# Kernel tuning notes

Hardware: AMD Instinct MI355X
Metric: run time of the kernel (lower is better)

## Reference

```python
import jax, jax.numpy as jnp
import numpy as np

N = 50000
E = 600000
F_IN = 128      # float features (in_channels - 1)
CE = 8          # cell embedding dim
D_IN = F_IN + CE  # 136
C = 128         # out_channels
NUM_CELLS = 854
NEG_SLOPE = 0.2
LN_EPS = 1e-5


def _gat_layer(x, src, dst, W, a_src, a_dst, b):
    """PyG GATConv, heads=1, concat=False, add_self_loops already in src/dst.
    x: [N, Din]; src/dst: [Etot]; W: [Din, C]; a_src/a_dst: [C]; b: [C].
    """
    h = x @ W                               # [N, C]
    alpha_src = h @ a_src                   # [N]
    alpha_dst = h @ a_dst                   # [N]
    e = jax.nn.leaky_relu(alpha_src[src] + alpha_dst[dst], NEG_SLOPE)  # [Etot]
    # segment softmax over edges sharing a destination node
    m = jax.ops.segment_max(e, dst, num_segments=N)    # [N] (every node has a self-loop)
    ex = jnp.exp(e - m[dst])                           # [Etot]
    denom = jax.ops.segment_sum(ex, dst, num_segments=N)  # [N]
    alpha = ex / denom[dst]                            # [Etot]
    out = jax.ops.segment_sum(h[src] * alpha[:, None], dst, num_segments=N)  # [N, C]
    return out + b


def _layer_norm(x, g, b):
    mu = jnp.mean(x, axis=-1, keepdims=True)
    var = jnp.var(x, axis=-1, keepdims=True)
    return (x - mu) * jax.lax.rsqrt(var + LN_EPS) * g + b


def setup_inputs() -> dict:
    key = jax.random.key(0)
    ks = jax.random.split(key, 12)
    x_base = jax.random.normal(ks[0], (N, F_IN), dtype=jnp.float32)
    cell_ids = jax.random.randint(ks[1], (N,), 0, NUM_CELLS, dtype=jnp.int64)
    edge_index = jax.random.randint(ks[2], (2, E), 0, N, dtype=jnp.int64)
    s = 0.05
    cell_emb = jax.random.normal(ks[3], (NUM_CELLS, CE), dtype=jnp.float32)
    W1 = jax.random.normal(ks[4], (D_IN, C), dtype=jnp.float32) * s
    a_src1 = jax.random.normal(ks[5], (C,), dtype=jnp.float32) * s
    a_dst1 = jax.random.normal(ks[6], (C,), dtype=jnp.float32) * s
    b1 = jnp.zeros((C,), dtype=jnp.float32)
    ln_g = jnp.ones((C,), dtype=jnp.float32)
    ln_b = jnp.zeros((C,), dtype=jnp.float32)
    W2 = jax.random.normal(ks[7], (C, C), dtype=jnp.float32) * s
    a_src2 = jax.random.normal(ks[8], (C,), dtype=jnp.float32) * s
    a_dst2 = jax.random.normal(ks[9], (C,), dtype=jnp.float32) * s
    b2 = jnp.zeros((C,), dtype=jnp.float32)
    return {
        "x_base": x_base, "cell_ids": cell_ids, "edge_index": edge_index,
        "cell_emb": cell_emb,
        "W1": W1, "a_src1": a_src1, "a_dst1": a_dst1, "b1": b1,
        "ln_g": ln_g, "ln_b": ln_b,
        "W2": W2, "a_src2": a_src2, "a_dst2": a_dst2, "b2": b2,
    }


def reference(x_base, cell_ids, edge_index, cell_emb,
              W1, a_src1, a_dst1, b1, ln_g, ln_b,
              W2, a_src2, a_dst2, b2):
    # embed cell ids and concat (equiv. to x[:, :-1] + Embedding(x[:, -1]))
    x = jnp.concatenate([x_base, cell_emb[cell_ids]], axis=1)   # [N, 136]
    # PyG GATConv adds self-loops internally
    loops = jnp.arange(N, dtype=edge_index.dtype)
    src = jnp.concatenate([edge_index[0], loops])
    dst = jnp.concatenate([edge_index[1], loops])
    # layer 1 + LN + ELU (dropout inactive in eval mode)
    x = _gat_layer(x, src, dst, W1, a_src1, a_dst1, b1)
    x = jax.nn.elu(_layer_norm(x, ln_g, ln_b))
    # layer 2 (no norm/activation on last layer)
    x = _gat_layer(x, src, dst, W2, a_src2, a_dst2, b2)
    return x
```

## Files before the change

### kernel.cpp

```cpp
#include <hip/hip_runtime.h>
#include <hip/hip_fp16.h>
#include <cstdint>
#include <cstddef>

#define NEG_SLOPE 0.2f
#define LN_EPS 1e-5f

constexpr int BS = 256;
constexpr int STRIDE = 96;

typedef _Float16 f16x8 __attribute__((ext_vector_type(8)));
typedef float f32x4 __attribute__((ext_vector_type(4)));

__global__ void k_build(
    const int* __restrict__ esrc, const int* __restrict__ edst,
    int* __restrict__ cnt, unsigned short* __restrict__ sn,
    const float* __restrict__ x, const int* __restrict__ cid,
    const float* __restrict__ emb, _Float16* __restrict__ xb,
    const float* __restrict__ W1, const float* __restrict__ W2,
    _Float16* __restrict__ Wt1, _Float16* __restrict__ Wt2,
    int e, int etot, int n, int npad, int nbE, int xblocks)
{
    int b = blockIdx.x;
    if (b < nbE) {
        int i = b * BS + threadIdx.x;
        if (i >= etot) return;
        int s, d;
        if (i < e) { s = esrc[i]; d = edst[i]; }
        else       { s = d = i - e; }
        int slot = atomicAdd(&cnt[d], 1);
        if (slot < STRIDE)
            sn[d * STRIDE + slot] = (unsigned short)s;
    } else if (b < nbE + xblocks) {
        int r = (b - nbE) * 8 + (threadIdx.x >> 5);
        int c = threadIdx.x & 31;
        if (r >= npad) return;
        _Float16* row = xb + (size_t)r * 160;
        if (r < n) {
            const float* xr = x + (size_t)r * 128;
            #pragma unroll
            for (int k = 0; k < 4; ++k) row[c + 32 * k] = (_Float16)xr[c + 32 * k];
            float v = (c < 8) ? emb[cid[r] * 8 + c] : 0.f;
            row[128 + c] = (_Float16)v;
        } else {
            #pragma unroll
            for (int k = 0; k < 5; ++k) row[c + 32 * k] = (_Float16)0.f;
        }
    } else {
        int idx = (b - nbE - xblocks) * BS + threadIdx.x;
        if (idx < 128 * 160) {
            int nn = idx / 160, k = idx - nn * 160;
            Wt1[idx] = (_Float16)((k < 136) ? W1[(size_t)k * 128 + nn] : 0.f);
        } else if (idx < 128 * 160 + 128 * 128) {
            int j = idx - 128 * 160;
            int nn = j >> 7, k = j & 127;
            Wt2[j] = (_Float16)W2[(size_t)k * 128 + nn];
        }
    }
}

template<int KP>
__global__ __launch_bounds__(256) void k_gemm_mfma(
    const _Float16* __restrict__ A, const _Float16* __restrict__ Bt,
    const float* __restrict__ a_src, const float* __restrict__ a_dst,
    _Float16* __restrict__ hb, float* __restrict__ as_,
    float* __restrict__ ad_, int n)
{
    __shared__ float red[2][16][2][2];
    int tid = threadIdx.x;
    int wave = tid >> 6, lane = tid & 63;
    int rg = wave >> 1, ch = wave & 1;
    int r15 = lane & 15, q = lane >> 4;
    int rowBase = blockIdx.x * 32 + rg * 16;
    int colBase = ch * 64;

    f32x4 acc[4] = {};

    const _Float16* Wp[4];
    #pragma unroll
    for (int s = 0; s < 4; ++s)
        Wp[s] = Bt + (size_t)(colBase + s * 16 + r15) * KP + q * 8;
    const _Float16* Xp = A + (size_t)(rowBase + r15) * KP + q * 8;

    #pragma unroll
    for (int k0 = 0; k0 < KP; k0 += 32) {
        f16x8 wv[4];
        #pragma unroll
        for (int s = 0; s < 4; ++s) wv[s] = *(const f16x8*)(Wp[s] + k0);
        f16x8 xv = *(const f16x8*)(Xp + k0);
        #pragma unroll
        for (int s = 0; s < 4; ++s)
            acc[s] = __builtin_amdgcn_mfma_f32_16x16x32_f16(wv[s], xv, acc[s], 0, 0, 0);
    }

    int row = rowBase + r15;
    bool ok = row < n;
    float vs = 0.f, vd = 0.f;
    #pragma unroll
    for (int s = 0; s < 4; ++s) {
        float4 as4 = *(const float4*)&a_src[colBase + s * 16 + q * 4];
        float4 ad4 = *(const float4*)&a_dst[colBase + s * 16 + q * 4];
        f32x4 d = acc[s];
        vs += d[0]*as4.x + d[1]*as4.y + d[2]*as4.z + d[3]*as4.w;
        vd += d[0]*ad4.x + d[1]*ad4.y + d[2]*ad4.z + d[3]*ad4.w;
        if (ok) {
            ushort4 u;
            u.x = __half_as_ushort(__float2half_rn(d[0]));
            u.y = __half_as_ushort(__float2half_rn(d[1]));
            u.z = __half_as_ushort(__float2half_rn(d[2]));
            u.w = __half_as_ushort(__float2half_rn(d[3]));
            *(ushort4*)&hb[(size_t)row * 128 + colBase + s * 16 + q * 4] = u;
        }
    }
    vs += __shfl_xor(vs, 16); vs += __shfl_xor(vs, 32);
    vd += __shfl_xor(vd, 16); vd += __shfl_xor(vd, 32);
    if (q == 0) { red[rg][r15][ch][0] = vs; red[rg][r15][ch][1] = vd; }
    __syncthreads();
    if (ch == 0 && q == 0 && ok) {
        as_[row] = red[rg][r15][0][0] + red[rg][r15][1][0];
        ad_[row] = red[rg][r15][0][1] + red[rg][r15][1][1];
    }
}

template<bool LN_ELU, bool OUT_HALF>
__global__ __launch_bounds__(256) void k_agg(
    const _Float16* __restrict__ hb, const unsigned short* __restrict__ sn,
    const int* __restrict__ cnt, const float* __restrict__ as_,
    const float* __restrict__ ad_, const float* __restrict__ bias,
    const float* __restrict__ ln_g, const float* __restrict__ ln_b,
    void* __restrict__ outv, int n_nodes)
{
    int wave = threadIdx.x >> 6, lane = threadIdx.x & 63;
    int n = blockIdx.x * 4 + wave;
    if (n >= n_nodes) return;
    int len = cnt[n];
    len = len < STRIDE ? len : STRIDE;
    len = __builtin_amdgcn_readfirstlane(len);
    int start = n * STRIDE;
    int l4 = lane & 15, q = lane >> 4;
    float adv = ad_[n];
    const char* hbB = (const char*)hb;

    float acc[8] = {0.f, 0.f, 0.f, 0.f, 0.f, 0.f, 0.f, 0.f};
    float dsum = 0.f;
    for (int j = 0; j < len; j += 16) {
        int rem = len - j;
        int offB = (l4 < rem) ? ((int)sn[start + j + l4] << 8) : 0;
        float t = as_[offB >> 8] + adv;
        t = t > 0.f ? t : NEG_SLOPE * t;
        float w0 = __expf(fminf(t, 70.f));
        #pragma unroll
        for (int v = 0; v < 4; ++v) {
            int e = 4 * v + q;
            int ob  = __shfl(offB, e);
            float w = __shfl(w0, e);
            if (e < rem) {
                f16x8 hv = *(const f16x8*)(hbB + ob + l4 * 16);
                #pragma unroll
                for (int c = 0; c < 8; ++c)
                    acc[c] = fmaf(w, (float)hv[c], acc[c]);
                dsum += w;
            }
        }
    }
    #pragma unroll
    for (int c = 0; c < 8; ++c) {
        acc[c] += __shfl_xor(acc[c], 16);
        acc[c] += __shfl_xor(acc[c], 32);
    }
    dsum += __shfl_xor(dsum, 16);
    dsum += __shfl_xor(dsum, 32);

    float inv = 1.f / dsum;
    float4 b0 = *(const float4*)&bias[l4 * 8];
    float4 b1 = *(const float4*)&bias[l4 * 8 + 4];
    float vv[8];
    vv[0] = acc[0] * inv + b0.x; vv[1] = acc[1] * inv + b0.y;
    vv[2] = acc[2] * inv + b0.z; vv[3] = acc[3] * inv + b0.w;
    vv[4] = acc[4] * inv + b1.x; vv[5] = acc[5] * inv + b1.y;
    vv[6] = acc[6] * inv + b1.z; vv[7] = acc[7] * inv + b1.w;

    if (LN_ELU) {
        float s1 = 0.f, s2 = 0.f;
        #pragma unroll
        for (int c = 0; c < 8; ++c) { s1 += vv[c]; s2 += vv[c] * vv[c]; }
        #pragma unroll
        for (int o = 1; o < 16; o <<= 1) {
            s1 += __shfl_xor(s1, o);
            s2 += __shfl_xor(s2, o);
        }
        float mean = s1 * (1.f / 128.f);
        float var  = s2 * (1.f / 128.f) - mean * mean;
        float r = rsqrtf(var + LN_EPS);
        float4 g0 = *(const float4*)&ln_g[l4 * 8];
        float4 g1 = *(const float4*)&ln_g[l4 * 8 + 4];
        float4 p0 = *(const float4*)&ln_b[l4 * 8];
        float4 p1 = *(const float4*)&ln_b[l4 * 8 + 4];
        float gg[8] = {g0.x, g0.y, g0.z, g0.w, g1.x, g1.y, g1.z, g1.w};
        float pp[8] = {p0.x, p0.y, p0.z, p0.w, p1.x, p1.y, p1.z, p1.w};
        #pragma unroll
        for (int c = 0; c < 8; ++c) {
            float t = (vv[c] - mean) * r * gg[c] + pp[c];
            vv[c] = t > 0.f ? t : __expf(t) - 1.f;
        }
    }

    if (q == 0) {
        if (OUT_HALF) {
            _Float16* out = (_Float16*)outv;
            f16x8 o;
            #pragma unroll
            for (int c = 0; c < 8; ++c) o[c] = (_Float16)vv[c];
            *(f16x8*)(out + (size_t)n * 128 + l4 * 8) = o;
        } else {
            float* out = (float*)outv;
            float4 o0 = make_float4(vv[0], vv[1], vv[2], vv[3]);
            float4 o1 = make_float4(vv[4], vv[5], vv[6], vv[7]);
            *(float4*)(out + (size_t)n * 128 + l4 * 8)     = o0;
            *(float4*)(out + (size_t)n * 128 + l4 * 8 + 4) = o1;
        }
    }
}


extern "C" void kernel_launch(void* const* d_in, const int* in_sizes, int n_in,
                              void* d_out, int out_size, void* d_ws, size_t ws_size,
                              hipStream_t stream) {
    const float* x_base   = (const float*)d_in[0];
    const int*   cell_ids = (const int*)d_in[1];
    const int*   eidx     = (const int*)d_in[2];
    const float* cell_emb = (const float*)d_in[3];
    const float* W1     = (const float*)d_in[4];
    const float* a_src1 = (const float*)d_in[5];
    const float* a_dst1 = (const float*)d_in[6];
    const float* b1     = (const float*)d_in[7];
    const float* ln_g   = (const float*)d_in[8];
    const float* ln_b   = (const float*)d_in[9];
    const float* W2     = (const float*)d_in[10];
    const float* a_src2 = (const float*)d_in[11];
    const float* a_dst2 = (const float*)d_in[12];
    const float* b2     = (const float*)d_in[13];

    const int N = in_sizes[0] / 128;
    const int E = in_sizes[2] / 2;
    const int ETOT = E + N;
    const int Npad  = ((N + 63) / 64) * 64;
    const int gridG = (N + 31) / 32;

    const int* esrc = eidx;
    const int* edst = eidx + E;

    auto align = [](size_t v) { return (v + 255) & ~(size_t)255; };
    char* p = (char*)d_ws;
    int*   cnt    = (int*)p;   p += align((size_t)N * 4);
    unsigned short* sn = (unsigned short*)p; p += align((size_t)N * STRIDE * 2 + 64);
    _Float16* xb  = (_Float16*)p; p += align((size_t)Npad * 160 * 2);
    _Float16* yb  = (_Float16*)p; p += align((size_t)Npad * 128 * 2);
    _Float16* hb  = (_Float16*)p; p += align((size_t)N * 128 * 2);
    _Float16* Wt1 = (_Float16*)p; p += align((size_t)128 * 160 * 2);
    _Float16* Wt2 = (_Float16*)p; p += align((size_t)128 * 128 * 2);
    float* as_    = (float*)p; p += align((size_t)N * 4);
    float* ad_    = (float*)p; p += align((size_t)N * 4);
    (void)ws_size; (void)n_in; (void)out_size;

    const int nbE = (ETOT + BS - 1) / BS;
    const int xblocks = (Npad + 7) / 8;
    const int wblocks = (128 * 160 + 128 * 128 + BS - 1) / BS;

    hipMemsetAsync(cnt, 0, (size_t)N * 4, stream);
    k_build<<<nbE + xblocks + wblocks, BS, 0, stream>>>(
        esrc, edst, cnt, sn,
        x_base, cell_ids, cell_emb, xb, W1, W2, Wt1, Wt2,
        E, ETOT, N, Npad, nbE, xblocks);

    k_gemm_mfma<160><<<gridG, 256, 0, stream>>>(xb, Wt1, a_src1, a_dst1, hb, as_, ad_, N);
    k_agg<true, true><<<(N + 3) / 4, 256, 0, stream>>>(
        hb, sn, cnt, as_, ad_, b1, ln_g, ln_b, (void*)yb, N);

    k_gemm_mfma<128><<<gridG, 256, 0, stream>>>(yb, Wt2, a_src2, a_dst2, hb, as_, ad_, N);
    k_agg<false, false><<<(N + 3) / 4, 256, 0, stream>>>(
        hb, sn, cnt, as_, ad_, b2, ln_g, ln_b, d_out, N);
}
```

Before: 244.1 us.

## Fuse all GAT stages into one persistent cooperative kernel with grid syncs

Replaces the memset plus five separate launches with a single cooperative persistent kernel. It runs init, CSR build with conversion, GEMM1, aggregation 1, GEMM2 and aggregation 2 as grid-stride phases separated by grid.sync(). Self-loops are now pre-seeded in an init phase instead of going through the atomic append. The aim is to remove launch gaps and the memset. In exchange it adds grid-wide barrier cost and a grid capped by occupancy, which may limit latency hiding in the gather-heavy aggregation. A multi-kernel fallback path is kept in case the cooperative launch fails.

```diff
diff --git a/kernel.cpp b/kernel.cpp
--- a/kernel.cpp
+++ b/kernel.cpp
@@ -1,4 +1,5 @@
 #include <hip/hip_runtime.h>
+#include <hip/hip_cooperative_groups.h>
 #include <hip/hip_fp16.h>
 #include <cstdint>
 #include <cstddef>
@@ -12,55 +13,23 @@
 typedef _Float16 f16x8 __attribute__((ext_vector_type(8)));
 typedef float f32x4 __attribute__((ext_vector_type(4)));
 
-__global__ void k_build(
-    const int* __restrict__ esrc, const int* __restrict__ edst,
-    int* __restrict__ cnt, unsigned short* __restrict__ sn,
-    const float* __restrict__ x, const int* __restrict__ cid,
-    const float* __restrict__ emb, _Float16* __restrict__ xb,
-    const float* __restrict__ W1, const float* __restrict__ W2,
-    _Float16* __restrict__ Wt1, _Float16* __restrict__ Wt2,
-    int e, int etot, int n, int npad, int nbE, int xblocks)
-{
-    int b = blockIdx.x;
-    if (b < nbE) {
-        int i = b * BS + threadIdx.x;
-        if (i >= etot) return;
-        int s, d;
-        if (i < e) { s = esrc[i]; d = edst[i]; }
-        else       { s = d = i - e; }
-        int slot = atomicAdd(&cnt[d], 1);
-        if (slot < STRIDE)
-            sn[d * STRIDE + slot] = (unsigned short)s;
-    } else if (b < nbE + xblocks) {
-        int r = (b - nbE) * 8 + (threadIdx.x >> 5);
-        int c = threadIdx.x & 31;
-        if (r >= npad) return;
-        _Float16* row = xb + (size_t)r * 160;
-        if (r < n) {
-            const float* xr = x + (size_t)r * 128;
-            #pragma unroll
-            for (int k = 0; k < 4; ++k) row[c + 32 * k] = (_Float16)xr[c + 32 * k];
-            float v = (c < 8) ? emb[cid[r] * 8 + c] : 0.f;
-            row[128 + c] = (_Float16)v;
-        } else {
-            #pragma unroll
-            for (int k = 0; k < 5; ++k) row[c + 32 * k] = (_Float16)0.f;
-        }
-    } else {
-        int idx = (b - nbE - xblocks) * BS + threadIdx.x;
-        if (idx < 128 * 160) {
-            int nn = idx / 160, k = idx - nn * 160;
-            Wt1[idx] = (_Float16)((k < 136) ? W1[(size_t)k * 128 + nn] : 0.f);
-        } else if (idx < 128 * 160 + 128 * 128) {
-            int j = idx - 128 * 160;
-            int nn = j >> 7, k = j & 127;
-            Wt2[j] = (_Float16)W2[(size_t)k * 128 + nn];
-        }
-    }
-}
+struct MegaArgs {
+    const int* esrc; const int* edst;
+    int* cnt; unsigned short* sn;
+    const float* x; const int* cid; const float* emb;
+    _Float16* xb;
+    const float* W1; const float* W2;
+    _Float16* Wt1; _Float16* Wt2;
+    const float* as1; const float* ad1; const float* b1;
+    const float* lng; const float* lnb;
+    const float* as2; const float* ad2; const float* b2;
+    _Float16* yb; _Float16* hb; float* fas; float* fad;
+    float* out;
+    int e, n, npad;
+};
 
 template<int KP>
-__global__ __launch_bounds__(256) void k_gemm_mfma(
+__device__ __forceinline__ void gemm_phase(
     const _Float16* __restrict__ A, const _Float16* __restrict__ Bt,
     const float* __restrict__ a_src, const float* __restrict__ a_dst,
     _Float16* __restrict__ hb, float* __restrict__ as_,
@@ -71,59 +40,63 @@
     int wave = tid >> 6, lane = tid & 63;
     int rg = wave >> 1, ch = wave & 1;
     int r15 = lane & 15, q = lane >> 4;
-    int rowBase = blockIdx.x * 32 + rg * 16;
     int colBase = ch * 64;
-
-    f32x4 acc[4] = {};
-
-    const _Float16* Wp[4];
-    #pragma unroll
-    for (int s = 0; s < 4; ++s)
-        Wp[s] = Bt + (size_t)(colBase + s * 16 + r15) * KP + q * 8;
-    const _Float16* Xp = A + (size_t)(rowBase + r15) * KP + q * 8;
-
-    #pragma unroll
-    for (int k0 = 0; k0 < KP; k0 += 32) {
-        f16x8 wv[4];
-        #pragma unroll
-        for (int s = 0; s < 4; ++s) wv[s] = *(const f16x8*)(Wp[s] + k0);
-        f16x8 xv = *(const f16x8*)(Xp + k0);
+    int nt = (n + 31) / 32;
+
+    for (int t = blockIdx.x; t < nt; t += gridDim.x) {
+        int rowBase = t * 32 + rg * 16;
+
+        f32x4 acc[4] = {};
+        const _Float16* Wp[4];
         #pragma unroll
         for (int s = 0; s < 4; ++s)
-            acc[s] = __builtin_amdgcn_mfma_f32_16x16x32_f16(wv[s], xv, acc[s], 0, 0, 0);
-    }
-
-    int row = rowBase + r15;
-    bool ok = row < n;
-    float vs = 0.f, vd = 0.f;
-    #pragma unroll
-    for (int s = 0; s < 4; ++s) {
-        float4 as4 = *(const float4*)&a_src[colBase + s * 16 + q * 4];
-        float4 ad4 = *(const float4*)&a_dst[colBase + s * 16 + q * 4];
-        f32x4 d = acc[s];
-        vs += d[0]*as4.x + d[1]*as4.y + d[2]*as4.z + d[3]*as4.w;
-        vd += d[0]*ad4.x + d[1]*ad4.y + d[2]*ad4.z + d[3]*ad4.w;
-        if (ok) {
-            ushort4 u;
-            u.x = __half_as_ushort(__float2half_rn(d[0]));
-            u.y = __half_as_ushort(__float2half_rn(d[1]));
-            u.z = __half_as_ushort(__float2half_rn(d[2]));
-            u.w = __half_as_ushort(__float2half_rn(d[3]));
-            *(ushort4*)&hb[(size_t)row * 128 + colBase + s * 16 + q * 4] = u;
-        }
-    }
-    vs += __shfl_xor(vs, 16); vs += __shfl_xor(vs, 32);
-    vd += __shfl_xor(vd, 16); vd += __shfl_xor(vd, 32);
-    if (q == 0) { red[rg][r15][ch][0] = vs; red[rg][r15][ch][1] = vd; }
-    __syncthreads();
-    if (ch == 0 && q == 0 && ok) {
-        as_[row] = red[rg][r15][0][0] + red[rg][r15][1][0];
-        ad_[row] = red[rg][r15][0][1] + red[rg][r15][1][1];
+            Wp[s] = Bt + (size_t)(colBase + s * 16 + r15) * KP + q * 8;
+        const _Float16* Xp = A + (size_t)(rowBase + r15) * KP + q * 8;
+
+        #pragma unroll
+        for (int k0 = 0; k0 < KP; k0 += 32) {
+            f16x8 wv[4];
+            #pragma unroll
+            for (int s = 0; s < 4; ++s) wv[s] = *(const f16x8*)(Wp[s] + k0);
+            f16x8 xv = *(const f16x8*)(Xp + k0);
+            #pragma unroll
+            for (int s = 0; s < 4; ++s)
+                acc[s] = __builtin_amdgcn_mfma_f32_16x16x32_f16(wv[s], xv, acc[s], 0, 0, 0);
+        }
+
+        int row = rowBase + r15;
+        bool ok = row < n;
+        float vs = 0.f, vd = 0.f;
+        #pragma unroll
+        for (int s = 0; s < 4; ++s) {
+            float4 as4 = *(const float4*)&a_src[colBase + s * 16 + q * 4];
+            float4 ad4 = *(const float4*)&a_dst[colBase + s * 16 + q * 4];
+            f32x4 d = acc[s];
+            vs += d[0]*as4.x + d[1]*as4.y + d[2]*as4.z + d[3]*as4.w;
+            vd += d[0]*ad4.x + d[1]*ad4.y + d[2]*ad4.z + d[3]*ad4.w;
+            if (ok) {
+                ushort4 u;
+                u.x = __half_as_ushort(__float2half_rn(d[0]));
+                u.y = __half_as_ushort(__float2half_rn(d[1]));
+                u.z = __half_as_ushort(__float2half_rn(d[2]));
+                u.w = __half_as_ushort(__float2half_rn(d[3]));
+                *(ushort4*)&hb[(size_t)row * 128 + colBase + s * 16 + q * 4] = u;
+            }
+        }
+        vs += __shfl_xor(vs, 16); vs += __shfl_xor(vs, 32);
+        vd += __shfl_xor(vd, 16); vd += __shfl_xor(vd, 32);
+        __syncthreads();
+        if (q == 0) { red[rg][r15][ch][0] = vs; red[rg][r15][ch][1] = vd; }
+        __syncthreads();
+        if (ch == 0 && q == 0 && ok) {
+            as_[row] = red[rg][r15][0][0] + red[rg][r15][1][0];
+            ad_[row] = red[rg][r15][0][1] + red[rg][r15][1][1];
+        }
     }
 }
 
 template<bool LN_ELU, bool OUT_HALF>
-__global__ __launch_bounds__(256) void k_agg(
+__device__ __forceinline__ void agg_phase(
     const _Float16* __restrict__ hb, const unsigned short* __restrict__ sn,
     const int* __restrict__ cnt, const float* __restrict__ as_,
     const float* __restrict__ ad_, const float* __restrict__ bias,
@@ -131,95 +104,179 @@
     void* __restrict__ outv, int n_nodes)
 {
     int wave = threadIdx.x >> 6, lane = threadIdx.x & 63;
-    int n = blockIdx.x * 4 + wave;
-    if (n >= n_nodes) return;
-    int len = cnt[n];
-    len = len < STRIDE ? len : STRIDE;
-    len = __builtin_amdgcn_readfirstlane(len);
-    int start = n * STRIDE;
     int l4 = lane & 15, q = lane >> 4;
-    float adv = ad_[n];
     const char* hbB = (const char*)hb;
-
-    float acc[8] = {0.f, 0.f, 0.f, 0.f, 0.f, 0.f, 0.f, 0.f};
-    float dsum = 0.f;
-    for (int j = 0; j < len; j += 16) {
-        int rem = len - j;
-        int offB = (l4 < rem) ? ((int)sn[start + j + l4] << 8) : 0;
-        float t = as_[offB >> 8] + adv;
-        t = t > 0.f ? t : NEG_SLOPE * t;
-        float w0 = __expf(fminf(t, 70.f));
-        #pragma unroll
-        for (int v = 0; v < 4; ++v) {
-            int e = 4 * v + q;
-            int ob  = __shfl(offB, e);
-            float w = __shfl(w0, e);
-            if (e < rem) {
-                f16x8 hv = *(const f16x8*)(hbB + ob + l4 * 16);
-                #pragma unroll
-                for (int c = 0; c < 8; ++c)
-                    acc[c] = fmaf(w, (float)hv[c], acc[c]);
-                dsum += w;
-            }
-        }
-    }
-    #pragma unroll
-    for (int c = 0; c < 8; ++c) {
-        acc[c] += __shfl_xor(acc[c], 16);
-        acc[c] += __shfl_xor(acc[c], 32);
-    }
-    dsum += __shfl_xor(dsum, 16);
-    dsum += __shfl_xor(dsum, 32);
-
-    float inv = 1.f / dsum;
-    float4 b0 = *(const float4*)&bias[l4 * 8];
-    float4 b1 = *(const float4*)&bias[l4 * 8 + 4];
-    float vv[8];
-    vv[0] = acc[0] * inv + b0.x; vv[1] = acc[1] * inv + b0.y;
-    vv[2] = acc[2] * inv + b0.z; vv[3] = acc[3] * inv + b0.w;
-    vv[4] = acc[4] * inv + b1.x; vv[5] = acc[5] * inv + b1.y;
-    vv[6] = acc[6] * inv + b1.z; vv[7] = acc[7] * inv + b1.w;
-
-    if (LN_ELU) {
-        float s1 = 0.f, s2 = 0.f;
-        #pragma unroll
-        for (int c = 0; c < 8; ++c) { s1 += vv[c]; s2 += vv[c] * vv[c]; }
-        #pragma unroll
-        for (int o = 1; o < 16; o <<= 1) {
-            s1 += __shfl_xor(s1, o);
-            s2 += __shfl_xor(s2, o);
-        }
-        float mean = s1 * (1.f / 128.f);
-        float var  = s2 * (1.f / 128.f) - mean * mean;
-        float r = rsqrtf(var + LN_EPS);
-        float4 g0 = *(const float4*)&ln_g[l4 * 8];
-        float4 g1 = *(const float4*)&ln_g[l4 * 8 + 4];
-        float4 p0 = *(const float4*)&ln_b[l4 * 8];
-        float4 p1 = *(const float4*)&ln_b[l4 * 8 + 4];
-        float gg[8] = {g0.x, g0.y, g0.z, g0.w, g1.x, g1.y, g1.z, g1.w};
-        float pp[8] = {p0.x, p0.y, p0.z, p0.w, p1.x, p1.y, p1.z, p1.w};
+    int ng = (n_nodes + 3) >> 2;
+
+    for (int g = blockIdx.x; g < ng; g += gridDim.x) {
+        int n = g * 4 + wave;
+        if (n >= n_nodes) continue;
+        int len = cnt[n];
+        len = len < STRIDE ? len : STRIDE;
+        len = __builtin_amdgcn_readfirstlane(len);
+        int start = n * STRIDE;
+        float adv = ad_[n];
+
+        float acc[8] = {0.f, 0.f, 0.f, 0.f, 0.f, 0.f, 0.f, 0.f};
+        float dsum = 0.f;
+        for (int j = 0; j < len; j += 16) {
+            int rem = len - j;
+            int offB = (l4 < rem) ? ((int)sn[start + j + l4] << 8) : 0;
+            float t = as_[offB >> 8] + adv;
+            t = t > 0.f ? t : NEG_SLOPE * t;
+            float w0 = __expf(fminf(t, 70.f));
+            #pragma unroll
+            for (int v = 0; v < 4; ++v) {
+                int e = 4 * v + q;
+                int ob  = __shfl(offB, e);
+                float w = __shfl(w0, e);
+                if (e < rem) {
+                    f16x8 hv = *(const f16x8*)(hbB + ob + l4 * 16);
+                    #pragma unroll
+                    for (int c = 0; c < 8; ++c)
+                        acc[c] = fmaf(w, (float)hv[c], acc[c]);
+                    dsum += w;
+                }
+            }
+        }
         #pragma unroll
         for (int c = 0; c < 8; ++c) {
-            float t = (vv[c] - mean) * r * gg[c] + pp[c];
-            vv[c] = t > 0.f ? t : __expf(t) - 1.f;
-        }
-    }
-
-    if (q == 0) {
-        if (OUT_HALF) {
-            _Float16* out = (_Float16*)outv;
-            f16x8 o;
-            #pragma unroll
-            for (int c = 0; c < 8; ++c) o[c] = (_Float16)vv[c];
-            *(f16x8*)(out + (size_t)n * 128 + l4 * 8) = o;
+            acc[c] += __shfl_xor(acc[c], 16);
+            acc[c] += __shfl_xor(acc[c], 32);
+        }
+        dsum += __shfl_xor(dsum, 16);
+        dsum += __shfl_xor(dsum, 32);
+
+        float inv = 1.f / dsum;
+        float4 b0 = *(const float4*)&bias[l4 * 8];
+        float4 b1 = *(const float4*)&bias[l4 * 8 + 4];
+        float vv[8];
+        vv[0] = acc[0] * inv + b0.x; vv[1] = acc[1] * inv + b0.y;
+        vv[2] = acc[2] * inv + b0.z; vv[3] = acc[3] * inv + b0.w;
+        vv[4] = acc[4] * inv + b1.x; vv[5] = acc[5] * inv + b1.y;
+        vv[6] = acc[6] * inv + b1.z; vv[7] = acc[7] * inv + b1.w;
+
+        if (LN_ELU) {
+            float s1 = 0.f, s2 = 0.f;
+            #pragma unroll
+            for (int c = 0; c < 8; ++c) { s1 += vv[c]; s2 += vv[c] * vv[c]; }
+            #pragma unroll
+            for (int o = 1; o < 16; o <<= 1) {
+                s1 += __shfl_xor(s1, o);
+                s2 += __shfl_xor(s2, o);
+            }
+            float mean = s1 * (1.f / 128.f);
+            float var  = s2 * (1.f / 128.f) - mean * mean;
+            float r = rsqrtf(var + LN_EPS);
+            float4 g0 = *(const float4*)&ln_g[l4 * 8];
+            float4 g1 = *(const float4*)&ln_g[l4 * 8 + 4];
+            float4 p0 = *(const float4*)&ln_b[l4 * 8];
+            float4 p1 = *(const float4*)&ln_b[l4 * 8 + 4];
+            float gg[8] = {g0.x, g0.y, g0.z, g0.w, g1.x, g1.y, g1.z, g1.w};
+            float pp[8] = {p0.x, p0.y, p0.z, p0.w, p1.x, p1.y, p1.z, p1.w};
+            #pragma unroll
+            for (int c = 0; c < 8; ++c) {
+                float t = (vv[c] - mean) * r * gg[c] + pp[c];
+                vv[c] = t > 0.f ? t : __expf(t) - 1.f;
+            }
+        }
+
+        if (q == 0) {
+            if (OUT_HALF) {
+                _Float16* out = (_Float16*)outv;
+                f16x8 o;
+                #pragma unroll
+                for (int c = 0; c < 8; ++c) o[c] = (_Float16)vv[c];
+                *(f16x8*)(out + (size_t)n * 128 + l4 * 8) = o;
+            } else {
+                float* out = (float*)outv;
+                float4 o0 = make_float4(vv[0], vv[1], vv[2], vv[3]);
+                float4 o1 = make_float4(vv[4], vv[5], vv[6], vv[7]);
+                *(float4*)(out + (size_t)n * 128 + l4 * 8)     = o0;
+                *(float4*)(out + (size_t)n * 128 + l4 * 8 + 4) = o1;
+            }
+        }
+    }
+}
+
+__device__ __forceinline__ void init_phase(MegaArgs& a, int gtid, int gsz) {
+    for (int i = gtid; i < a.n; i += gsz) {
+        a.cnt[i] = 1;
+        a.sn[(size_t)i * STRIDE] = (unsigned short)i;
+    }
+}
+
+__device__ __forceinline__ void build_phase(MegaArgs& a, int gtid, int gsz) {
+    for (int i = gtid; i < a.e; i += gsz) {
+        int s = a.esrc[i], d = a.edst[i];
+        int slot = atomicAdd(&a.cnt[d], 1);
+        if (slot < STRIDE)
+            a.sn[(size_t)d * STRIDE + slot] = (unsigned short)s;
+    }
+    {
+        int c = gtid & 31;
+        for (int r = gtid >> 5; r < a.npad; r += gsz >> 5) {
+            _Float16* row = a.xb + (size_t)r * 160;
+            if (r < a.n) {
+                const float* xr = a.x + (size_t)r * 128;
+                #pragma unroll
+                for (int k = 0; k < 4; ++k) row[c + 32 * k] = (_Float16)xr[c + 32 * k];
+                float v = (c < 8) ? a.emb[a.cid[r] * 8 + c] : 0.f;
+                row[128 + c] = (_Float16)v;
+            } else {
+                #pragma unroll
+                for (int k = 0; k < 5; ++k) row[c + 32 * k] = (_Float16)0.f;
+            }
+        }
+    }
+    for (int idx = gtid; idx < 128 * 160 + 128 * 128; idx += gsz) {
+        if (idx < 128 * 160) {
+            int nn = idx / 160, k = idx - nn * 160;
+            a.Wt1[idx] = (_Float16)((k < 136) ? a.W1[(size_t)k * 128 + nn] : 0.f);
         } else {
-            float* out = (float*)outv;
-            float4 o0 = make_float4(vv[0], vv[1], vv[2], vv[3]);
-            float4 o1 = make_float4(vv[4], vv[5], vv[6], vv[7]);
-            *(float4*)(out + (size_t)n * 128 + l4 * 8)     = o0;
-            *(float4*)(out + (size_t)n * 128 + l4 * 8 + 4) = o1;
-        }
-    }
+            int j = idx - 128 * 160;
+            int nn = j >> 7, k = j & 127;
+            a.Wt2[j] = (_Float16)a.W2[(size_t)k * 128 + nn];
+        }
+    }
+}
+
+__global__ void __launch_bounds__(256, 4) k_mega(MegaArgs a)
+{
+    cooperative_groups::grid_group grid = cooperative_groups::this_grid();
+    const int gsz  = gridDim.x * BS;
+    const int gtid = blockIdx.x * BS + threadIdx.x;
+
+    init_phase(a, gtid, gsz);
+    grid.sync();
+    build_phase(a, gtid, gsz);
+    grid.sync();
+    gemm_phase<160>(a.xb, a.Wt1, a.as1, a.ad1, a.hb, a.fas, a.fad, a.n);
+    grid.sync();
+    agg_phase<true, true>(a.hb, a.sn, a.cnt, a.fas, a.fad, a.b1, a.lng, a.lnb, (void*)a.yb, a.n);
+    grid.sync();
+    gemm_phase<128>(a.yb, a.Wt2, a.as2, a.ad2, a.hb, a.fas, a.fad, a.n);
+    grid.sync();
+    agg_phase<false, false>(a.hb, a.sn, a.cnt, a.fas, a.fad, a.b2, a.lng, a.lnb, (void*)a.out, a.n);
+}
+
+__global__ void __launch_bounds__(256) kf_init(MegaArgs a) {
+    init_phase(a, blockIdx.x * BS + threadIdx.x, gridDim.x * BS);
+}
+__global__ void __launch_bounds__(256) kf_build(MegaArgs a) {
+    build_phase(a, blockIdx.x * BS + threadIdx.x, gridDim.x * BS);
+}
+__global__ void __launch_bounds__(256) kf_gemm1(MegaArgs a) {
+    gemm_phase<160>(a.xb, a.Wt1, a.as1, a.ad1, a.hb, a.fas, a.fad, a.n);
+}
+__global__ void __launch_bounds__(256) kf_agg1(MegaArgs a) {
+    agg_phase<true, true>(a.hb, a.sn, a.cnt, a.fas, a.fad, a.b1, a.lng, a.lnb, (void*)a.yb, a.n);
+}
+__global__ void __launch_bounds__(256) kf_gemm2(MegaArgs a) {
+    gemm_phase<128>(a.yb, a.Wt2, a.as2, a.ad2, a.hb, a.fas, a.fad, a.n);
+}
+__global__ void __launch_bounds__(256) kf_agg2(MegaArgs a) {
+    agg_phase<false, false>(a.hb, a.sn, a.cnt, a.fas, a.fad, a.b2, a.lng, a.lnb, (void*)a.out, a.n);
 }
 
 
@@ -243,12 +300,7 @@
 
     const int N = in_sizes[0] / 128;
     const int E = in_sizes[2] / 2;
-    const int ETOT = E + N;
-    const int Npad  = ((N + 63) / 64) * 64;
-    const int gridG = (N + 31) / 32;
-
-    const int* esrc = eidx;
-    const int* edst = eidx + E;
+    const int Npad = ((N + 63) / 64) * 64;
 
     auto align = [](size_t v) { return (v + 255) & ~(size_t)255; };
     char* p = (char*)d_ws;
@@ -263,21 +315,43 @@
     float* ad_    = (float*)p; p += align((size_t)N * 4);
     (void)ws_size; (void)n_in; (void)out_size;
 
-    const int nbE = (ETOT + BS - 1) / BS;
-    const int xblocks = (Npad + 7) / 8;
-    const int wblocks = (128 * 160 + 128 * 128 + BS - 1) / BS;
-
-    hipMemsetAsync(cnt, 0, (size_t)N * 4, stream);
-    k_build<<<nbE + xblocks + wblocks, BS, 0, stream>>>(
-        esrc, edst, cnt, sn,
-        x_base, cell_ids, cell_emb, xb, W1, W2, Wt1, Wt2,
-        E, ETOT, N, Npad, nbE, xblocks);
-
-    k_gemm_mfma<160><<<gridG, 256, 0, stream>>>(xb, Wt1, a_src1, a_dst1, hb, as_, ad_, N);
-    k_agg<true, true><<<(N + 3) / 4, 256, 0, stream>>>(
-        hb, sn, cnt, as_, ad_, b1, ln_g, ln_b, (void*)yb, N);
-
-    k_gemm_mfma<128><<<gridG, 256, 0, stream>>>(yb, Wt2, a_src2, a_dst2, hb, as_, ad_, N);
-    k_agg<false, false><<<(N + 3) / 4, 256, 0, stream>>>(
-        hb, sn, cnt, as_, ad_, b2, ln_g, ln_b, d_out, N);
-}
+    MegaArgs a;
+    a.esrc = eidx; a.edst = eidx + E;
+    a.cnt = cnt; a.sn = sn;
+    a.x = x_base; a.cid = cell_ids; a.emb = cell_emb;
+    a.xb = xb;
+    a.W1 = W1; a.W2 = W2; a.Wt1 = Wt1; a.Wt2 = Wt2;
+    a.as1 = a_src1; a.ad1 = a_dst1; a.b1 = b1;
+    a.lng = ln_g; a.lnb = ln_b;
+    a.as2 = a_src2; a.ad2 = a_dst2; a.b2 = b2;
+    a.yb = yb; a.hb = hb; a.fas = as_; a.fad = ad_;
+    a.out = (float*)d_out;
+    a.e = E; a.n = N; a.npad = Npad;
+
+    static int s_grid = 0;
+    if (s_grid == 0) {
+        int nb = 0;
+        if (hipOccupancyMaxActiveBlocksPerMultiprocessor(&nb, k_mega, BS, 0) != hipSuccess || nb < 1)
+            nb = 4;
+        int dev = 0, cu = 0;
+        hipGetDevice(&dev);
+        if (hipDeviceGetAttribute(&cu, hipDeviceAttributeMultiprocessorCount, dev) != hipSuccess || cu < 1)
+            cu = 256;
+        long g = (long)nb * cu;
+        s_grid = (int)(g > 2048 ? 2048 : g);
+    }
+
+    void* kargs[] = { (void*)&a };
+    hipError_t err = hipLaunchCooperativeKernel((const void*)k_mega, dim3(s_grid), dim3(BS),
+                                                kargs, 0, stream);
+    if (err != hipSuccess) {
+        const int nbN = (N + BS - 1) / BS;
+        const int nbE = (E + BS - 1) / BS;
+        kf_init <<<nbN, BS, 0, stream>>>(a);
+        kf_build<<<nbE, BS, 0, stream>>>(a);
+        kf_gemm1<<<(N + 31) / 32, BS, 0, stream>>>(a);
+        kf_agg1 <<<(N + 3) / 4, BS, 0, stream>>>(a);
+        kf_gemm2<<<(N + 31) / 32, BS, 0, stream>>>(a);
+        kf_agg2 <<<(N + 3) / 4, BS, 0, stream>>>(a);
+    }
+}
```

Result: slower. 667.8 us (+173.6%).

## Fuse edge scatter with GEMM1 and aggregation1 with GEMM2, drop staging buffers

Applied to the files above, without the earlier changes.

Restructures the pipeline from memset plus five launches into four kernels. The memset is replaced by an init kernel that seeds self-loops. Edge scatter now runs in the same launch as layer-1 GEMM, with blocks interleaved, and that GEMM reads fp32 x and the cell embedding directly instead of a prebuilt fp16 padded copy. Layer-1 aggregation with LN+ELU is fused with the layer-2 GEMM through a shared-memory tile, so the fp16 intermediate round trip and separate launches go away. In exchange, the agg1 blocks process 32 nodes with four waves each looping serially over 8 nodes, which lowers parallelism and may unbalance degree-dependent work.

```diff
diff --git a/kernel.cpp b/kernel.cpp
--- a/kernel.cpp
+++ b/kernel.cpp
@@ -12,42 +12,18 @@
 typedef _Float16 f16x8 __attribute__((ext_vector_type(8)));
 typedef float f32x4 __attribute__((ext_vector_type(4)));
 
-__global__ void k_build(
-    const int* __restrict__ esrc, const int* __restrict__ edst,
+__global__ __launch_bounds__(256) void k_init(
     int* __restrict__ cnt, unsigned short* __restrict__ sn,
-    const float* __restrict__ x, const int* __restrict__ cid,
-    const float* __restrict__ emb, _Float16* __restrict__ xb,
     const float* __restrict__ W1, const float* __restrict__ W2,
     _Float16* __restrict__ Wt1, _Float16* __restrict__ Wt2,
-    int e, int etot, int n, int npad, int nbE, int xblocks)
+    int n, int nbN)
 {
     int b = blockIdx.x;
-    if (b < nbE) {
+    if (b < nbN) {
         int i = b * BS + threadIdx.x;
-        if (i >= etot) return;
-        int s, d;
-        if (i < e) { s = esrc[i]; d = edst[i]; }
-        else       { s = d = i - e; }
-        int slot = atomicAdd(&cnt[d], 1);
-        if (slot < STRIDE)
-            sn[d * STRIDE + slot] = (unsigned short)s;
-    } else if (b < nbE + xblocks) {
-        int r = (b - nbE) * 8 + (threadIdx.x >> 5);
-        int c = threadIdx.x & 31;
-        if (r >= npad) return;
-        _Float16* row = xb + (size_t)r * 160;
-        if (r < n) {
-            const float* xr = x + (size_t)r * 128;
-            #pragma unroll
-            for (int k = 0; k < 4; ++k) row[c + 32 * k] = (_Float16)xr[c + 32 * k];
-            float v = (c < 8) ? emb[cid[r] * 8 + c] : 0.f;
-            row[128 + c] = (_Float16)v;
-        } else {
-            #pragma unroll
-            for (int k = 0; k < 5; ++k) row[c + 32 * k] = (_Float16)0.f;
-        }
+        if (i < n) { cnt[i] = 1; sn[(size_t)i * STRIDE] = (unsigned short)i; }
     } else {
-        int idx = (b - nbE - xblocks) * BS + threadIdx.x;
+        int idx = (b - nbN) * BS + threadIdx.x;
         if (idx < 128 * 160) {
             int nn = idx / 160, k = idx - nn * 160;
             Wt1[idx] = (_Float16)((k < 136) ? W1[(size_t)k * 128 + nn] : 0.f);
@@ -59,42 +35,89 @@
     }
 }
 
-template<int KP>
-__global__ __launch_bounds__(256) void k_gemm_mfma(
-    const _Float16* __restrict__ A, const _Float16* __restrict__ Bt,
+__global__ __launch_bounds__(256) void k_scatter_gemm1(
+    const int* __restrict__ esrc, const int* __restrict__ edst,
+    int* __restrict__ cnt, unsigned short* __restrict__ sn,
+    const float* __restrict__ x, const int* __restrict__ cid,
+    const float* __restrict__ emb,
+    const _Float16* __restrict__ Wt1,
     const float* __restrict__ a_src, const float* __restrict__ a_dst,
-    _Float16* __restrict__ hb, float* __restrict__ as_,
-    float* __restrict__ ad_, int n)
+    _Float16* __restrict__ hb, float* __restrict__ as_, float* __restrict__ ad_,
+    int e, int n, int nbG, int nbA)
 {
     __shared__ float red[2][16][2][2];
+    int b = blockIdx.x;
+    int role, idx;
+    int nInter = 2 * (nbG < nbA ? nbG : nbA);
+    if (b < nInter)      { role = b & 1; idx = b >> 1; }
+    else if (nbG < nbA)  { role = 1; idx = (b - nInter) + nbG; }
+    else                 { role = 0; idx = (b - nInter) + nbA; }
+
+    if (role == 1) {
+        int i = idx * BS + threadIdx.x;
+        if (i < e) {
+            int s = esrc[i], d = edst[i];
+            int slot = atomicAdd(&cnt[d], 1);
+            if (slot < STRIDE)
+                sn[(size_t)d * STRIDE + slot] = (unsigned short)s;
+        }
+        return;
+    }
+
     int tid = threadIdx.x;
     int wave = tid >> 6, lane = tid & 63;
     int rg = wave >> 1, ch = wave & 1;
     int r15 = lane & 15, q = lane >> 4;
-    int rowBase = blockIdx.x * 32 + rg * 16;
+    int rowBase = idx * 32 + rg * 16;
     int colBase = ch * 64;
+    int row = rowBase + r15;
+    bool ok = row < n;
+    int rl = ok ? row : n - 1;
 
     f32x4 acc[4] = {};
-
     const _Float16* Wp[4];
     #pragma unroll
     for (int s = 0; s < 4; ++s)
-        Wp[s] = Bt + (size_t)(colBase + s * 16 + r15) * KP + q * 8;
-    const _Float16* Xp = A + (size_t)(rowBase + r15) * KP + q * 8;
-
-    #pragma unroll
-    for (int k0 = 0; k0 < KP; k0 += 32) {
+        Wp[s] = Wt1 + (size_t)(colBase + s * 16 + r15) * 160 + q * 8;
+    const float* Xp = x + (size_t)rl * 128 + q * 8;
+
+    #pragma unroll
+    for (int k0 = 0; k0 < 128; k0 += 32) {
         f16x8 wv[4];
         #pragma unroll
         for (int s = 0; s < 4; ++s) wv[s] = *(const f16x8*)(Wp[s] + k0);
-        f16x8 xv = *(const f16x8*)(Xp + k0);
+        float4 xlo = *(const float4*)(Xp + k0);
+        float4 xhi = *(const float4*)(Xp + k0 + 4);
+        f16x8 xv;
+        xv[0] = (_Float16)xlo.x; xv[1] = (_Float16)xlo.y;
+        xv[2] = (_Float16)xlo.z; xv[3] = (_Float16)xlo.w;
+        xv[4] = (_Float16)xhi.x; xv[5] = (_Float16)xhi.y;
+        xv[6] = (_Float16)xhi.z; xv[7] = (_Float16)xhi.w;
         #pragma unroll
         for (int s = 0; s < 4; ++s)
             acc[s] = __builtin_amdgcn_mfma_f32_16x16x32_f16(wv[s], xv, acc[s], 0, 0, 0);
     }
-
-    int row = rowBase + r15;
-    bool ok = row < n;
+    {
+        f16x8 wv[4];
+        #pragma unroll
+        for (int s = 0; s < 4; ++s) wv[s] = *(const f16x8*)(Wp[s] + 128);
+        f16x8 xv;
+        #pragma unroll
+        for (int j = 0; j < 8; ++j) xv[j] = (_Float16)0.f;
+        if (q == 0) {
+            const float* er = emb + (size_t)cid[rl] * 8;
+            float4 e0 = *(const float4*)er;
+            float4 e1 = *(const float4*)(er + 4);
+            xv[0] = (_Float16)e0.x; xv[1] = (_Float16)e0.y;
+            xv[2] = (_Float16)e0.z; xv[3] = (_Float16)e0.w;
+            xv[4] = (_Float16)e1.x; xv[5] = (_Float16)e1.y;
+            xv[6] = (_Float16)e1.z; xv[7] = (_Float16)e1.w;
+        }
+        #pragma unroll
+        for (int s = 0; s < 4; ++s)
+            acc[s] = __builtin_amdgcn_mfma_f32_16x16x32_f16(wv[s], xv, acc[s], 0, 0, 0);
+    }
+
     float vs = 0.f, vd = 0.f;
     #pragma unroll
     for (int s = 0; s < 4; ++s) {
@@ -122,13 +145,161 @@
     }
 }
 
-template<bool LN_ELU, bool OUT_HALF>
-__global__ __launch_bounds__(256) void k_agg(
+__global__ __launch_bounds__(256) void k_agg1_gemm2(
+    const _Float16* __restrict__ h1, const unsigned short* __restrict__ sn,
+    const int* __restrict__ cnt, const float* __restrict__ as1,
+    const float* __restrict__ ad1, const float* __restrict__ b1,
+    const float* __restrict__ lng, const float* __restrict__ lnb,
+    const _Float16* __restrict__ Wt2,
+    const float* __restrict__ a_src2, const float* __restrict__ a_dst2,
+    _Float16* __restrict__ h2, float* __restrict__ as2, float* __restrict__ ad2,
+    int nn)
+{
+    __shared__ _Float16 yt[32][144];
+    __shared__ float red[2][16][2][2];
+    int t = blockIdx.x;
+    int tid = threadIdx.x;
+    int wave = tid >> 6, lane = tid & 63;
+    int l4 = lane & 15, q = lane >> 4;
+    const char* hbB = (const char*)h1;
+
+    for (int i = 0; i < 8; ++i) {
+        int node = t * 32 + wave * 8 + i;
+        if (node >= nn) break;
+        int len = cnt[node];
+        len = len < STRIDE ? len : STRIDE;
+        len = __builtin_amdgcn_readfirstlane(len);
+        int start = node * STRIDE;
+        float adv = ad1[node];
+
+        float acc[8] = {0.f, 0.f, 0.f, 0.f, 0.f, 0.f, 0.f, 0.f};
+        float dsum = 0.f;
+        for (int j = 0; j < len; j += 16) {
+            int rem = len - j;
+            int offB = (l4 < rem) ? ((int)sn[start + j + l4] << 8) : 0;
+            float tt = as1[offB >> 8] + adv;
+            tt = tt > 0.f ? tt : NEG_SLOPE * tt;
+            float w0 = __expf(fminf(tt, 70.f));
+            #pragma unroll
+            for (int v = 0; v < 4; ++v) {
+                int e = 4 * v + q;
+                int ob  = __shfl(offB, e);
+                float w = __shfl(w0, e);
+                if (e < rem) {
+                    f16x8 hv = *(const f16x8*)(hbB + ob + l4 * 16);
+                    #pragma unroll
+                    for (int c = 0; c < 8; ++c)
+                        acc[c] = fmaf(w, (float)hv[c], acc[c]);
+                    dsum += w;
+                }
+            }
+        }
+        #pragma unroll
+        for (int c = 0; c < 8; ++c) {
+            acc[c] += __shfl_xor(acc[c], 16);
+            acc[c] += __shfl_xor(acc[c], 32);
+        }
+        dsum += __shfl_xor(dsum, 16);
+        dsum += __shfl_xor(dsum, 32);
+
+        float inv = 1.f / dsum;
+        float4 b0 = *(const float4*)&b1[l4 * 8];
+        float4 bb = *(const float4*)&b1[l4 * 8 + 4];
+        float vv[8];
+        vv[0] = acc[0] * inv + b0.x; vv[1] = acc[1] * inv + b0.y;
+        vv[2] = acc[2] * inv + b0.z; vv[3] = acc[3] * inv + b0.w;
+        vv[4] = acc[4] * inv + bb.x; vv[5] = acc[5] * inv + bb.y;
+        vv[6] = acc[6] * inv + bb.z; vv[7] = acc[7] * inv + bb.w;
+
+        float s1 = 0.f, s2 = 0.f;
+        #pragma unroll
+        for (int c = 0; c < 8; ++c) { s1 += vv[c]; s2 += vv[c] * vv[c]; }
+        #pragma unroll
+        for (int o = 1; o < 16; o <<= 1) {
+            s1 += __shfl_xor(s1, o);
+            s2 += __shfl_xor(s2, o);
+        }
+        float mean = s1 * (1.f / 128.f);
+        float var  = s2 * (1.f / 128.f) - mean * mean;
+        float r = rsqrtf(var + LN_EPS);
+        float4 g0 = *(const float4*)&lng[l4 * 8];
+        float4 g1 = *(const float4*)&lng[l4 * 8 + 4];
+        float4 p0 = *(const float4*)&lnb[l4 * 8];
+        float4 p1 = *(const float4*)&lnb[l4 * 8 + 4];
+        float gg[8] = {g0.x, g0.y, g0.z, g0.w, g1.x, g1.y, g1.z, g1.w};
+        float pp[8] = {p0.x, p0.y, p0.z, p0.w, p1.x, p1.y, p1.z, p1.w};
+        #pragma unroll
+        for (int c = 0; c < 8; ++c) {
+            float u = (vv[c] - mean) * r * gg[c] + pp[c];
+            vv[c] = u > 0.f ? u : __expf(u) - 1.f;
+        }
+
+        if (q == 0) {
+            f16x8 o;
+            #pragma unroll
+            for (int c = 0; c < 8; ++c) o[c] = (_Float16)vv[c];
+            *(f16x8*)&yt[wave * 8 + i][l4 * 8] = o;
+        }
+    }
+    __syncthreads();
+
+    int rg = wave >> 1, ch = wave & 1;
+    int r15 = lane & 15;
+    int rowBase = t * 32 + rg * 16;
+    int colBase = ch * 64;
+    int row = rowBase + r15;
+    bool ok = row < nn;
+
+    f32x4 acc2[4] = {};
+    const _Float16* Wp[4];
+    #pragma unroll
+    for (int s = 0; s < 4; ++s)
+        Wp[s] = Wt2 + (size_t)(colBase + s * 16 + r15) * 128 + q * 8;
+    const _Float16* Yp = &yt[rg * 16 + r15][q * 8];
+
+    #pragma unroll
+    for (int k0 = 0; k0 < 128; k0 += 32) {
+        f16x8 wv[4];
+        #pragma unroll
+        for (int s = 0; s < 4; ++s) wv[s] = *(const f16x8*)(Wp[s] + k0);
+        f16x8 xv = *(const f16x8*)(Yp + k0);
+        #pragma unroll
+        for (int s = 0; s < 4; ++s)
+            acc2[s] = __builtin_amdgcn_mfma_f32_16x16x32_f16(wv[s], xv, acc2[s], 0, 0, 0);
+    }
+
+    float vs = 0.f, vd = 0.f;
+    #pragma unroll
+    for (int s = 0; s < 4; ++s) {
+        float4 as4 = *(const float4*)&a_src2[colBase + s * 16 + q * 4];
+        float4 ad4 = *(const float4*)&a_dst2[colBase + s * 16 + q * 4];
+        f32x4 d = acc2[s];
+        vs += d[0]*as4.x + d[1]*as4.y + d[2]*as4.z + d[3]*as4.w;
+        vd += d[0]*ad4.x + d[1]*ad4.y + d[2]*ad4.z + d[3]*ad4.w;
+        if (ok) {
+            ushort4 u;
+            u.x = __half_as_ushort(__float2half_rn(d[0]));
+            u.y = __half_as_ushort(__float2half_rn(d[1]));
+            u.z = __half_as_ushort(__float2half_rn(d[2]));
+            u.w = __half_as_ushort(__float2half_rn(d[3]));
+            *(ushort4*)&h2[(size_t)row * 128 + colBase + s * 16 + q * 4] = u;
+        }
+    }
+    vs += __shfl_xor(vs, 16); vs += __shfl_xor(vs, 32);
+    vd += __shfl_xor(vd, 16); vd += __shfl_xor(vd, 32);
+    if (q == 0) { red[rg][r15][ch][0] = vs; red[rg][r15][ch][1] = vd; }
+    __syncthreads();
+    if (ch == 0 && q == 0 && ok) {
+        as2[row] = red[rg][r15][0][0] + red[rg][r15][1][0];
+        ad2[row] = red[rg][r15][0][1] + red[rg][r15][1][1];
+    }
+}
+
+__global__ __launch_bounds__(256) void k_agg2(
     const _Float16* __restrict__ hb, const unsigned short* __restrict__ sn,
     const int* __restrict__ cnt, const float* __restrict__ as_,
     const float* __restrict__ ad_, const float* __restrict__ bias,
-    const float* __restrict__ ln_g, const float* __restrict__ ln_b,
-    void* __restrict__ outv, int n_nodes)
+    float* __restrict__ out, int n_nodes)
 {
     int wave = threadIdx.x >> 6, lane = threadIdx.x & 63;
     int n = blockIdx.x * 4 + wave;
@@ -171,54 +342,16 @@
     dsum += __shfl_xor(dsum, 16);
     dsum += __shfl_xor(dsum, 32);
 
-    float inv = 1.f / dsum;
-    float4 b0 = *(const float4*)&bias[l4 * 8];
-    float4 b1 = *(const float4*)&bias[l4 * 8 + 4];
-    float vv[8];
-    vv[0] = acc[0] * inv + b0.x; vv[1] = acc[1] * inv + b0.y;
-    vv[2] = acc[2] * inv + b0.z; vv[3] = acc[3] * inv + b0.w;
-    vv[4] = acc[4] * inv + b1.x; vv[5] = acc[5] * inv + b1.y;
-    vv[6] = acc[6] * inv + b1.z; vv[7] = acc[7] * inv + b1.w;
-
-    if (LN_ELU) {
-        float s1 = 0.f, s2 = 0.f;
-        #pragma unroll
-        for (int c = 0; c < 8; ++c) { s1 += vv[c]; s2 += vv[c] * vv[c]; }
-        #pragma unroll
-        for (int o = 1; o < 16; o <<= 1) {
-            s1 += __shfl_xor(s1, o);
-            s2 += __shfl_xor(s2, o);
-        }
-        float mean = s1 * (1.f / 128.f);
-        float var  = s2 * (1.f / 128.f) - mean * mean;
-        float r = rsqrtf(var + LN_EPS);
-        float4 g0 = *(const float4*)&ln_g[l4 * 8];
-        float4 g1 = *(const float4*)&ln_g[l4 * 8 + 4];
-        float4 p0 = *(const float4*)&ln_b[l4 * 8];
-        float4 p1 = *(const float4*)&ln_b[l4 * 8 + 4];
-        float gg[8] = {g0.x, g0.y, g0.z, g0.w, g1.x, g1.y, g1.z, g1.w};
-        float pp[8] = {p0.x, p0.y, p0.z, p0.w, p1.x, p1.y, p1.z, p1.w};
-        #pragma unroll
-        for (int c = 0; c < 8; ++c) {
-            float t = (vv[c] - mean) * r * gg[c] + pp[c];
-            vv[c] = t > 0.f ? t : __expf(t) - 1.f;
-        }
-    }
-
     if (q == 0) {
-        if (OUT_HALF) {
-            _Float16* out = (_Float16*)outv;
-            f16x8 o;
-            #pragma unroll
-            for (int c = 0; c < 8; ++c) o[c] = (_Float16)vv[c];
-            *(f16x8*)(out + (size_t)n * 128 + l4 * 8) = o;
-        } else {
-            float* out = (float*)outv;
-            float4 o0 = make_float4(vv[0], vv[1], vv[2], vv[3]);
-            float4 o1 = make_float4(vv[4], vv[5], vv[6], vv[7]);
-            *(float4*)(out + (size_t)n * 128 + l4 * 8)     = o0;
-            *(float4*)(out + (size_t)n * 128 + l4 * 8 + 4) = o1;
-        }
+        float inv = 1.f / dsum;
+        float4 b0 = *(const float4*)&bias[l4 * 8];
+        float4 b1 = *(const float4*)&bias[l4 * 8 + 4];
+        float4 o0 = make_float4(acc[0]*inv + b0.x, acc[1]*inv + b0.y,
+                                acc[2]*inv + b0.z, acc[3]*inv + b0.w);
+        float4 o1 = make_float4(acc[4]*inv + b1.x, acc[5]*inv + b1.y,
+                                acc[6]*inv + b1.z, acc[7]*inv + b1.w);
+        *(float4*)(out + (size_t)n * 128 + l4 * 8)     = o0;
+        *(float4*)(out + (size_t)n * 128 + l4 * 8 + 4) = o1;
     }
 }
 
@@ -243,9 +376,6 @@
 
     const int N = in_sizes[0] / 128;
     const int E = in_sizes[2] / 2;
-    const int ETOT = E + N;
-    const int Npad  = ((N + 63) / 64) * 64;
-    const int gridG = (N + 31) / 32;
 
     const int* esrc = eidx;
     const int* edst = eidx + E;
@@ -254,30 +384,28 @@
     char* p = (char*)d_ws;
     int*   cnt    = (int*)p;   p += align((size_t)N * 4);
     unsigned short* sn = (unsigned short*)p; p += align((size_t)N * STRIDE * 2 + 64);
-    _Float16* xb  = (_Float16*)p; p += align((size_t)Npad * 160 * 2);
-    _Float16* yb  = (_Float16*)p; p += align((size_t)Npad * 128 * 2);
-    _Float16* hb  = (_Float16*)p; p += align((size_t)N * 128 * 2);
+    _Float16* h1  = (_Float16*)p; p += align((size_t)N * 128 * 2);
+    _Float16* h2  = (_Float16*)p; p += align((size_t)N * 128 * 2);
     _Float16* Wt1 = (_Float16*)p; p += align((size_t)128 * 160 * 2);
     _Float16* Wt2 = (_Float16*)p; p += align((size_t)128 * 128 * 2);
-    float* as_    = (float*)p; p += align((size_t)N * 4);
-    float* ad_    = (float*)p; p += align((size_t)N * 4);
+    float* as1    = (float*)p; p += align((size_t)N * 4);
+    float* ad1    = (float*)p; p += align((size_t)N * 4);
+    float* as2    = (float*)p; p += align((size_t)N * 4);
+    float* ad2    = (float*)p; p += align((size_t)N * 4);
     (void)ws_size; (void)n_in; (void)out_size;
 
-    const int nbE = (ETOT + BS - 1) / BS;
-    const int xblocks = (Npad + 7) / 8;
+    const int nbN = (N + BS - 1) / BS;
+    const int nbA = (E + BS - 1) / BS;
+    const int nbG = (N + 31) / 32;
     const int wblocks = (128 * 160 + 128 * 128 + BS - 1) / BS;
 
-    hipMemsetAsync(cnt, 0, (size_t)N * 4, stream);
-    k_build<<<nbE + xblocks + wblocks, BS, 0, stream>>>(
-        esrc, edst, cnt, sn,
-        x_base, cell_ids, cell_emb, xb, W1, W2, Wt1, Wt2,
-        E, ETOT, N, Npad, nbE, xblocks);
-
-    k_gemm_mfma<160><<<gridG, 256, 0, stream>>>(xb, Wt1, a_src1, a_dst1, hb, as_, ad_, N);
-    k_agg<true, true><<<(N + 3) / 4, 256, 0, stream>>>(
-        hb, sn, cnt, as_, ad_, b1, ln_g, ln_b, (void*)yb, N);
-
-    k_gemm_mfma<128><<<gridG, 256, 0, stream>>>(yb, Wt2, a_src2, a_dst2, hb, as_, ad_, N);
-    k_agg<false, false><<<(N + 3) / 4, 256, 0, stream>>>(
-        hb, sn, cnt, as_, ad_, b2, ln_g, ln_b, d_out, N);
+    k_init<<<nbN + wblocks, BS, 0, stream>>>(cnt, sn, W1, W2, Wt1, Wt2, N, nbN);
+    k_scatter_gemm1<<<nbG + nbA, BS, 0, stream>>>(
+        esrc, edst, cnt, sn, x_base, cell_ids, cell_emb, Wt1,
+        a_src1, a_dst1, h1, as1, ad1, E, N, nbG, nbA);
+    k_agg1_gemm2<<<nbG, BS, 0, stream>>>(
+        h1, sn, cnt, as1, ad1, b1, ln_g, ln_b, Wt2,
+        a_src2, a_dst2, h2, as2, ad2, N);
+    k_agg2<<<(N + 3) / 4, BS, 0, stream>>>(
+        h2, sn, cnt, as2, ad2, b2, (float*)d_out, N);
 }
```

Result: no change. 242.1 us (-0.8%).
